# Kernel optimization log

Hardware: AMD Instinct MI355X
Metric: run time of the kernel (lower is better)

The kernel has to match this reference:

```python
import jax, jax.numpy as jnp
import numpy as np

CAUSAL = True


def setup_inputs() -> dict:
    key = jax.random.key(0)
    k1, k2, k3 = jax.random.split(key, 3)
    B, H, T, D = 2, 16, 2048, 64
    q = jax.random.normal(k1, (B, H, T, D), dtype=jnp.float32)
    k = jax.random.normal(k2, (B, H, T, D), dtype=jnp.float32)
    v = jax.random.normal(k3, (B, H, T, D), dtype=jnp.float32)
    return {"q": q, "k": k, "v": v}


def reference(q, k, v):
    # q,k,v: [B,H,T,D]
    d = q.shape[-1]
    scale = d ** -0.5
    dots = jnp.einsum('bhid,bhjd->bhij', q, k) * scale  # [B,H,T,T]
    if CAUSAL:
        t = q.shape[2]
        mask = jnp.triu(jnp.ones((t, t), dtype=bool), k=1)  # True above diagonal
        dots = jnp.where(mask, -jnp.inf, dots)
    attn = jax.nn.softmax(dots, axis=-1)
    # torch.einsum('bhjd,bhij->bhid', v, attn) == attn @ v
    return jnp.einsum('bhij,bhjd->bhid', attn, v)
```

## Files before the change

### kernel.cpp

```cpp
#include <hip/hip_runtime.h>
#include <hip/hip_bf16.h>

typedef unsigned short u16;
typedef unsigned int u32;
typedef __bf16 bf16x8 __attribute__((ext_vector_type(8)));
typedef short s16x4 __attribute__((ext_vector_type(4)));
typedef short s16x8 __attribute__((ext_vector_type(8)));
typedef float floatx4 __attribute__((ext_vector_type(4)));

#define T_SEQ 2048
#define HDIM 64
#define NBH 32

static __device__ __forceinline__ u16 f2b_rne(float x) {
    union { float f; u32 u; } c; c.f = x;
    u32 u = c.u;
    return (u16)((u + 0x7fffu + ((u >> 16) & 1u)) >> 16);
}
static __device__ __forceinline__ u16 f2b_trunc(float x) {
    union { float f; u32 u; } c; c.f = x;
    return (u16)(c.u >> 16);
}

#define GLOAD_LDS16(gp, lp)                                                      \
    __builtin_amdgcn_global_load_lds(                                            \
        (const __attribute__((address_space(1))) u32*)(gp),                      \
        (__attribute__((address_space(3))) u32*)(lp), 16, 0, 0)

__global__ __launch_bounds__(256) void prep(const float* __restrict__ k,
                                            const float* __restrict__ v,
                                            u16* __restrict__ kb,
                                            u16* __restrict__ vt) {
    __shared__ u16 tile[64][68];
    const int bh = blockIdx.y, t0 = blockIdx.x * 64;
    const int tid = threadIdx.x;

    const float* ksrc = k + ((size_t)bh * T_SEQ + t0) * HDIM;
    u16* kdst = kb + ((size_t)bh * T_SEQ + t0) * HDIM;
#pragma unroll
    for (int p = 0; p < 4; p++) {
        int idx = p * 256 + tid;
        float4 f = ((const float4*)ksrc)[idx];
        ushort4 o;
        o.x = f2b_rne(f.x); o.y = f2b_rne(f.y); o.z = f2b_rne(f.z); o.w = f2b_rne(f.w);
        ((ushort4*)kdst)[idx] = o;
    }

    const float* vsrc = v + ((size_t)bh * T_SEQ + t0) * HDIM;
#pragma unroll
    for (int p = 0; p < 4; p++) {
        int idx = p * 256 + tid;
        int r = idx >> 4, c4 = (idx & 15) * 4;
        float4 f = *(const float4*)(vsrc + r * HDIM + c4);
        tile[c4 + 0][r] = f2b_rne(f.x);
        tile[c4 + 1][r] = f2b_rne(f.y);
        tile[c4 + 2][r] = f2b_rne(f.z);
        tile[c4 + 3][r] = f2b_rne(f.w);
    }
    __syncthreads();
    u16* dst = vt + (size_t)bh * HDIM * T_SEQ + t0;
#pragma unroll
    for (int p = 0; p < 4; p++) {
        int idx = p * 256 + tid;
        int d = idx >> 4, c4 = (idx & 15) * 4;
        int win = c4 >> 5, kt = (c4 >> 4) & 1, qg = (c4 >> 2) & 3;
        int pos = win * 32 + qg * 8 + kt * 4;
        *(ushort4*)(dst + (size_t)d * T_SEQ + pos) = *(ushort4*)(&tile[d][c4]);
    }
}

__global__ __launch_bounds__(256, 2) void fattn(const float* __restrict__ q,
                                                const u16* __restrict__ kb,
                                                const u16* __restrict__ vtb,
                                                float* __restrict__ out) {
    __shared__ __align__(16) u16 smem[35328];

    const int bh = blockIdx.x;
    const int qt = 31 - (int)blockIdx.y;
    const int tid = threadIdx.x;
    const int wave = tid >> 6, lane = tid & 63;
    const int l15 = lane & 15, quad = lane >> 4;

    const float* qp = q + (size_t)bh * T_SEQ * HDIM;
    const u16* kp = kb + (size_t)bh * T_SEQ * HDIM;
    const u16* vp = vtb + (size_t)bh * HDIM * T_SEQ;

    const int nwin = 2 * qt + 2;
    const int nmy = (nwin > wave) ? ((nwin - wave + 3) >> 2) : 0;

    u16* Tb = smem + wave * 8192;

    const int ln3 = lane >> 3, ln7 = lane & 7;
    const int ln2 = lane >> 2, ln3m = lane & 3;

    auto stage = [&](int win, int b) {
        const u16* ks = kp + win * 32 * HDIM;
        u16* Kd = Tb + b * 2048;
#pragma unroll
        for (int l = 0; l < 4; l++) {
            int kr = l * 8 + ln3;
            GLOAD_LDS16(ks + kr * HDIM + (ln7 ^ (kr & 7)) * 8, Kd + l * 512);
        }
        const u16* vs = vp + win * 32;
        u16* Vd = Tb + 4096 + b * 2048;
#pragma unroll
        for (int l = 0; l < 4; l++) {
            int dr = l * 16 + ln2;
            GLOAD_LDS16(vs + (size_t)dr * T_SEQ + ((ln3m - dr) & 3) * 8, Vd + l * 512);
        }
    };

    const float SL2E = 0.125f * 1.44269504088896f;
    bf16x8 qf[4][2];
#pragma unroll
    for (int qn = 0; qn < 4; qn++) {
        const float* qrow = qp + (size_t)(qt * 64 + qn * 16 + l15) * HDIM;
#pragma unroll
        for (int kc = 0; kc < 2; kc++) {
            const float4* p4 = (const float4*)(qrow + kc * 32 + quad * 8);
            float4 fa = p4[0], fb = p4[1];
            union { bf16x8 v; u16 s[8]; } cv;
            cv.s[0] = f2b_rne(fa.x * SL2E); cv.s[1] = f2b_rne(fa.y * SL2E);
            cv.s[2] = f2b_rne(fa.z * SL2E); cv.s[3] = f2b_rne(fa.w * SL2E);
            cv.s[4] = f2b_rne(fb.x * SL2E); cv.s[5] = f2b_rne(fb.y * SL2E);
            cv.s[6] = f2b_rne(fb.z * SL2E); cv.s[7] = f2b_rne(fb.w * SL2E);
            qf[qn][kc] = cv.v;
        }
    }
    asm volatile("s_waitcnt vmcnt(0)" ::: "memory");

    if (nmy > 0) stage(wave, 0);
    if (nmy > 1) stage(wave + 4, 1);

    floatx4 o_acc[4][4];
#pragma unroll
    for (int qn = 0; qn < 4; qn++)
#pragma unroll
        for (int dt = 0; dt < 4; dt++) o_acc[qn][dt] = (floatx4){0.f, 0.f, 0.f, 0.f};
    float lsum[4] = {0.f, 0.f, 0.f, 0.f};

    for (int i = 0; i < nmy; i++) {
        const int win = wave + 4 * i;
        const int b = i & 1;
        if (i + 1 < nmy) { asm volatile("s_waitcnt vmcnt(8)" ::: "memory"); }
        else             { asm volatile("s_waitcnt vmcnt(0)" ::: "memory"); }

        const u16* Kc = Tb + b * 2048;
        bf16x8 kf[2][2];
#pragma unroll
        for (int kt = 0; kt < 2; kt++) {
            int kr = kt * 16 + l15;
#pragma unroll
            for (int kc = 0; kc < 2; kc++)
                kf[kt][kc] = *(const bf16x8*)(Kc + kr * 64 + (((kc * 4 + quad) ^ (kr & 7)) * 8));
        }
        const u16* Vc = Tb + 4096 + b * 2048;
        s16x8 vfull[4];
#pragma unroll
        for (int dt = 0; dt < 4; dt++) {
            int d = dt * 16 + l15;
            vfull[dt] = *(const s16x8*)(Vc + d * 32 + ((quad + d) & 3) * 8);
        }
        asm volatile("s_waitcnt lgkmcnt(0)" ::: "memory");
        if (i + 2 < nmy) stage(wave + 4 * (i + 2), b);

        floatx4 sacc[2][4];
#pragma unroll
        for (int kt = 0; kt < 2; kt++)
#pragma unroll
            for (int qn = 0; qn < 4; qn++) sacc[kt][qn] = (floatx4){0.f, 0.f, 0.f, 0.f};
#pragma unroll
        for (int kc = 0; kc < 2; kc++)
#pragma unroll
            for (int kt = 0; kt < 2; kt++)
#pragma unroll
                for (int qn = 0; qn < 4; qn++)
                    sacc[kt][qn] = __builtin_amdgcn_mfma_f32_16x16x32_bf16(
                        kf[kt][kc], qf[qn][kc], sacc[kt][qn], 0, 0, 0);

        s16x4 pf[2][4];
        if (win >= 2 * qt) {
            const int base = (win - 2 * qt) * 32;
#pragma unroll
            for (int kt = 0; kt < 2; kt++)
#pragma unroll
                for (int qn = 0; qn < 4; qn++) {
                    union { s16x4 v; u16 h[4]; } pk;
#pragma unroll
                    for (int rg = 0; rg < 4; rg++) {
                        float e = __builtin_amdgcn_exp2f(sacc[kt][qn][rg]);
                        if (base + kt * 16 + quad * 4 + rg > qn * 16 + l15) e = 0.f;
                        lsum[qn] += e;
                        pk.h[rg] = f2b_trunc(e);
                    }
                    pf[kt][qn] = pk.v;
                }
        } else {
#pragma unroll
            for (int kt = 0; kt < 2; kt++)
#pragma unroll
                for (int qn = 0; qn < 4; qn++) {
                    union { s16x4 v; u16 h[4]; } pk;
#pragma unroll
                    for (int rg = 0; rg < 4; rg++) {
                        float e = __builtin_amdgcn_exp2f(sacc[kt][qn][rg]);
                        lsum[qn] += e;
                        pk.h[rg] = f2b_trunc(e);
                    }
                    pf[kt][qn] = pk.v;
                }
        }

#pragma unroll
        for (int dt = 0; dt < 4; dt++) {
            s16x4 v0 = __builtin_shufflevector(vfull[dt], vfull[dt], 0, 1, 2, 3);
            s16x4 v1 = __builtin_shufflevector(vfull[dt], vfull[dt], 4, 5, 6, 7);
#pragma unroll
            for (int qn = 0; qn < 4; qn++) {
                o_acc[qn][dt] = __builtin_amdgcn_mfma_f32_16x16x16bf16_1k(pf[0][qn], v0, o_acc[qn][dt], 0, 0, 0);
                o_acc[qn][dt] = __builtin_amdgcn_mfma_f32_16x16x16bf16_1k(pf[1][qn], v1, o_acc[qn][dt], 0, 0, 0);
            }
        }
    }

    __syncthreads();
    float* oq = (float*)smem + wave * 4352;
#pragma unroll
    for (int qn = 0; qn < 4; qn++)
#pragma unroll
        for (int dt = 0; dt < 4; dt++)
#pragma unroll
            for (int rg = 0; rg < 4; rg++)
                oq[(qn * 16 + quad * 4 + rg) * 68 + dt * 16 + l15] = o_acc[qn][dt][rg];

    float* lsa = (float*)smem + 17408;
#pragma unroll
    for (int qn = 0; qn < 4; qn++) {
        float t = lsum[qn];
        t += __shfl_xor(t, 16, 64);
        t += __shfl_xor(t, 32, 64);
        if (quad == 0) lsa[wave * 64 + qn * 16 + l15] = t;
    }
    __syncthreads();

    {
        const int qr = wave * 16 + l15;
        float lt = lsa[qr] + lsa[64 + qr] + lsa[128 + qr] + lsa[192 + qr];
        float inv = 1.0f / lt;
        const float* q0 = (float*)smem + qr * 68 + quad * 16;
        float* op = out + ((size_t)bh * T_SEQ + qt * 64 + qr) * HDIM + quad * 16;
#pragma unroll
        for (int c = 0; c < 4; c++) {
            float4 s0 = *(const float4*)(q0 + c * 4);
            float4 s1 = *(const float4*)(q0 + 4352 + c * 4);
            float4 s2 = *(const float4*)(q0 + 8704 + c * 4);
            float4 s3 = *(const float4*)(q0 + 13056 + c * 4);
            float4 r;
            r.x = (s0.x + s1.x + s2.x + s3.x) * inv;
            r.y = (s0.y + s1.y + s2.y + s3.y) * inv;
            r.z = (s0.z + s1.z + s2.z + s3.z) * inv;
            r.w = (s0.w + s1.w + s2.w + s3.w) * inv;
            *(float4*)(op + c * 4) = r;
        }
    }
}

extern "C" void kernel_launch(void* const* d_in, const int* in_sizes, int n_in,
                              void* d_out, int out_size, void* d_ws, size_t ws_size,
                              hipStream_t stream) {
    const float* q = (const float*)d_in[0];
    const float* k = (const float*)d_in[1];
    const float* v = (const float*)d_in[2];
    float* out = (float*)d_out;

    u16* kb = (u16*)d_ws;
    u16* vt = kb + (size_t)NBH * T_SEQ * HDIM;

    prep<<<dim3(T_SEQ / 64, NBH), 256, 0, stream>>>(k, v, kb, vt);
    fattn<<<dim3(NBH, 32), 256, 0, stream>>>(q, kb, vt, out);
}
```

Baseline: 124.2 us.

## Shrink per-wave KV windows to 16 keys and cut LDS for higher occupancy

```diff
diff --git a/kernel.cpp b/kernel.cpp
--- a/kernel.cpp
+++ b/kernel.cpp
@@ -5,7 +5,6 @@
 typedef unsigned int u32;
 typedef __bf16 bf16x8 __attribute__((ext_vector_type(8)));
 typedef short s16x4 __attribute__((ext_vector_type(4)));
-typedef short s16x8 __attribute__((ext_vector_type(8)));
 typedef float floatx4 __attribute__((ext_vector_type(4)));
 
 #define T_SEQ 2048
@@ -17,9 +16,9 @@
     u32 u = c.u;
     return (u16)((u + 0x7fffu + ((u >> 16) & 1u)) >> 16);
 }
-static __device__ __forceinline__ u16 f2b_trunc(float x) {
+static __device__ __forceinline__ u32 fbits(float x) {
     union { float f; u32 u; } c; c.f = x;
-    return (u16)(c.u >> 16);
+    return c.u;
 }
 
 #define GLOAD_LDS16(gp, lp)                                                      \
@@ -63,17 +62,15 @@
     for (int p = 0; p < 4; p++) {
         int idx = p * 256 + tid;
         int d = idx >> 4, c4 = (idx & 15) * 4;
-        int win = c4 >> 5, kt = (c4 >> 4) & 1, qg = (c4 >> 2) & 3;
-        int pos = win * 32 + qg * 8 + kt * 4;
-        *(ushort4*)(dst + (size_t)d * T_SEQ + pos) = *(ushort4*)(&tile[d][c4]);
-    }
-}
-
-__global__ __launch_bounds__(256, 2) void fattn(const float* __restrict__ q,
+        *(ushort4*)(dst + (size_t)d * T_SEQ + c4) = *(ushort4*)(&tile[d][c4]);
+    }
+}
+
+__global__ __launch_bounds__(256, 3) void fattn(const float* __restrict__ q,
                                                 const u16* __restrict__ kb,
                                                 const u16* __restrict__ vtb,
                                                 float* __restrict__ out) {
-    __shared__ __align__(16) u16 smem[35328];
+    __shared__ __align__(16) u16 smem[18944];
 
     const int bh = blockIdx.x;
     const int qt = 31 - (int)blockIdx.y;
@@ -85,29 +82,22 @@
     const u16* kp = kb + (size_t)bh * T_SEQ * HDIM;
     const u16* vp = vtb + (size_t)bh * HDIM * T_SEQ;
 
-    const int nwin = 2 * qt + 2;
-    const int nmy = (nwin > wave) ? ((nwin - wave + 3) >> 2) : 0;
-
-    u16* Tb = smem + wave * 8192;
-
-    const int ln3 = lane >> 3, ln7 = lane & 7;
-    const int ln2 = lane >> 2, ln3m = lane & 3;
+    u16* Tb = smem + wave * 4096;
+
+    const int kr = lane >> 3;
+    const u16* kg0 = kp + kr * HDIM + ((lane & 7) ^ (kr & 7)) * 8;
+    const int vdr = lane >> 1;
+    const u16* vg0 = vp + (size_t)vdr * T_SEQ + (((lane & 1) + (vdr >> 2)) & 1) * 8;
 
     auto stage = [&](int win, int b) {
-        const u16* ks = kp + win * 32 * HDIM;
-        u16* Kd = Tb + b * 2048;
-#pragma unroll
-        for (int l = 0; l < 4; l++) {
-            int kr = l * 8 + ln3;
-            GLOAD_LDS16(ks + kr * HDIM + (ln7 ^ (kr & 7)) * 8, Kd + l * 512);
-        }
-        const u16* vs = vp + win * 32;
-        u16* Vd = Tb + 4096 + b * 2048;
-#pragma unroll
-        for (int l = 0; l < 4; l++) {
-            int dr = l * 16 + ln2;
-            GLOAD_LDS16(vs + (size_t)dr * T_SEQ + ((ln3m - dr) & 3) * 8, Vd + l * 512);
-        }
+        const u16* ks = kg0 + win * 16 * HDIM;
+        u16* Kd = Tb + b * 1024;
+        GLOAD_LDS16(ks, Kd);
+        GLOAD_LDS16(ks + 8 * HDIM, Kd + 512);
+        const u16* vs = vg0 + win * 16;
+        u16* Vd = Tb + 2048 + b * 1024;
+        GLOAD_LDS16(vs, Vd);
+        GLOAD_LDS16(vs + (size_t)32 * T_SEQ, Vd + 512);
     };
 
     const float SL2E = 0.125f * 1.44269504088896f;
@@ -129,8 +119,8 @@
     }
     asm volatile("s_waitcnt vmcnt(0)" ::: "memory");
 
-    if (nmy > 0) stage(wave, 0);
-    if (nmy > 1) stage(wave + 4, 1);
+    stage(wave, 0);
+    if (qt >= 1) stage(wave + 4, 1);
 
     floatx4 o_acc[4][4];
 #pragma unroll
@@ -138,102 +128,87 @@
 #pragma unroll
         for (int dt = 0; dt < 4; dt++) o_acc[qn][dt] = (floatx4){0.f, 0.f, 0.f, 0.f};
     float lsum[4] = {0.f, 0.f, 0.f, 0.f};
-
-    for (int i = 0; i < nmy; i++) {
-        const int win = wave + 4 * i;
+    const floatx4 ZERO4 = {0.f, 0.f, 0.f, 0.f};
+    const int vph = ((quad >> 1) + (l15 >> 2)) & 1;
+
+    for (int i = 0; i <= qt; ++i) {
         const int b = i & 1;
-        if (i + 1 < nmy) { asm volatile("s_waitcnt vmcnt(8)" ::: "memory"); }
-        else             { asm volatile("s_waitcnt vmcnt(0)" ::: "memory"); }
-
-        const u16* Kc = Tb + b * 2048;
-        bf16x8 kf[2][2];
-#pragma unroll
-        for (int kt = 0; kt < 2; kt++) {
-            int kr = kt * 16 + l15;
-#pragma unroll
-            for (int kc = 0; kc < 2; kc++)
-                kf[kt][kc] = *(const bf16x8*)(Kc + kr * 64 + (((kc * 4 + quad) ^ (kr & 7)) * 8));
-        }
-        const u16* Vc = Tb + 4096 + b * 2048;
-        s16x8 vfull[4];
-#pragma unroll
-        for (int dt = 0; dt < 4; dt++) {
-            int d = dt * 16 + l15;
-            vfull[dt] = *(const s16x8*)(Vc + d * 32 + ((quad + d) & 3) * 8);
-        }
+        if (i < qt) { asm volatile("s_waitcnt vmcnt(4)" ::: "memory"); }
+        else        { asm volatile("s_waitcnt vmcnt(0)" ::: "memory"); }
+
+        const u16* Kc = Tb + b * 1024;
+        bf16x8 kf0 = *(const bf16x8*)(Kc + l15 * 64 + ((quad) ^ (l15 & 7)) * 8);
+        bf16x8 kf1 = *(const bf16x8*)(Kc + l15 * 64 + ((4 + quad) ^ (l15 & 7)) * 8);
+        const u16* Vc = Tb + 2048 + b * 1024;
+        s16x4 vf[4];
+#pragma unroll
+        for (int dt = 0; dt < 4; dt++)
+            vf[dt] = *(const s16x4*)(Vc + (dt * 16 + l15) * 16 + vph * 8 + (quad & 1) * 4);
         asm volatile("s_waitcnt lgkmcnt(0)" ::: "memory");
-        if (i + 2 < nmy) stage(wave + 4 * (i + 2), b);
-
-        floatx4 sacc[2][4];
-#pragma unroll
-        for (int kt = 0; kt < 2; kt++)
-#pragma unroll
-            for (int qn = 0; qn < 4; qn++) sacc[kt][qn] = (floatx4){0.f, 0.f, 0.f, 0.f};
-#pragma unroll
-        for (int kc = 0; kc < 2; kc++)
-#pragma unroll
-            for (int kt = 0; kt < 2; kt++)
-#pragma unroll
-                for (int qn = 0; qn < 4; qn++)
-                    sacc[kt][qn] = __builtin_amdgcn_mfma_f32_16x16x32_bf16(
-                        kf[kt][kc], qf[qn][kc], sacc[kt][qn], 0, 0, 0);
-
-        s16x4 pf[2][4];
-        if (win >= 2 * qt) {
-            const int base = (win - 2 * qt) * 32;
-#pragma unroll
-            for (int kt = 0; kt < 2; kt++)
-#pragma unroll
-                for (int qn = 0; qn < 4; qn++) {
-                    union { s16x4 v; u16 h[4]; } pk;
-#pragma unroll
-                    for (int rg = 0; rg < 4; rg++) {
-                        float e = __builtin_amdgcn_exp2f(sacc[kt][qn][rg]);
-                        if (base + kt * 16 + quad * 4 + rg > qn * 16 + l15) e = 0.f;
-                        lsum[qn] += e;
-                        pk.h[rg] = f2b_trunc(e);
-                    }
-                    pf[kt][qn] = pk.v;
-                }
+        if (i + 2 <= qt) stage(wave + 4 * (i + 2), b);
+
+        floatx4 sacc[4];
+#pragma unroll
+        for (int qn = 0; qn < 4; qn++)
+            sacc[qn] = __builtin_amdgcn_mfma_f32_16x16x32_bf16(kf0, qf[qn][0], ZERO4, 0, 0, 0);
+#pragma unroll
+        for (int qn = 0; qn < 4; qn++)
+            sacc[qn] = __builtin_amdgcn_mfma_f32_16x16x32_bf16(kf1, qf[qn][1], sacc[qn], 0, 0, 0);
+
+        s16x4 pf[4];
+        if (i == qt) {
+#pragma unroll
+            for (int qn = 0; qn < 4; qn++) {
+                const int rhs = qn * 16 + l15;
+                float e0 = __builtin_amdgcn_exp2f(sacc[qn][0]);
+                float e1 = __builtin_amdgcn_exp2f(sacc[qn][1]);
+                float e2 = __builtin_amdgcn_exp2f(sacc[qn][2]);
+                float e3 = __builtin_amdgcn_exp2f(sacc[qn][3]);
+                if (wave * 16 + quad * 4 + 0 > rhs) e0 = 0.f;
+                if (wave * 16 + quad * 4 + 1 > rhs) e1 = 0.f;
+                if (wave * 16 + quad * 4 + 2 > rhs) e2 = 0.f;
+                if (wave * 16 + quad * 4 + 3 > rhs) e3 = 0.f;
+                lsum[qn] += (e0 + e1) + (e2 + e3);
+                union { s16x4 v; u32 w[2]; } pk;
+                pk.w[0] = __builtin_amdgcn_perm(fbits(e1), fbits(e0), 0x07060302u);
+                pk.w[1] = __builtin_amdgcn_perm(fbits(e3), fbits(e2), 0x07060302u);
+                pf[qn] = pk.v;
+            }
         } else {
 #pragma unroll
-            for (int kt = 0; kt < 2; kt++)
-#pragma unroll
-                for (int qn = 0; qn < 4; qn++) {
-                    union { s16x4 v; u16 h[4]; } pk;
-#pragma unroll
-                    for (int rg = 0; rg < 4; rg++) {
-                        float e = __builtin_amdgcn_exp2f(sacc[kt][qn][rg]);
-                        lsum[qn] += e;
-                        pk.h[rg] = f2b_trunc(e);
-                    }
-                    pf[kt][qn] = pk.v;
-                }
-        }
-
-#pragma unroll
-        for (int dt = 0; dt < 4; dt++) {
-            s16x4 v0 = __builtin_shufflevector(vfull[dt], vfull[dt], 0, 1, 2, 3);
-            s16x4 v1 = __builtin_shufflevector(vfull[dt], vfull[dt], 4, 5, 6, 7);
-#pragma unroll
             for (int qn = 0; qn < 4; qn++) {
-                o_acc[qn][dt] = __builtin_amdgcn_mfma_f32_16x16x16bf16_1k(pf[0][qn], v0, o_acc[qn][dt], 0, 0, 0);
-                o_acc[qn][dt] = __builtin_amdgcn_mfma_f32_16x16x16bf16_1k(pf[1][qn], v1, o_acc[qn][dt], 0, 0, 0);
+                float e0 = __builtin_amdgcn_exp2f(sacc[qn][0]);
+                float e1 = __builtin_amdgcn_exp2f(sacc[qn][1]);
+                float e2 = __builtin_amdgcn_exp2f(sacc[qn][2]);
+                float e3 = __builtin_amdgcn_exp2f(sacc[qn][3]);
+                lsum[qn] += (e0 + e1) + (e2 + e3);
+                union { s16x4 v; u32 w[2]; } pk;
+                pk.w[0] = __builtin_amdgcn_perm(fbits(e1), fbits(e0), 0x07060302u);
+                pk.w[1] = __builtin_amdgcn_perm(fbits(e3), fbits(e2), 0x07060302u);
+                pf[qn] = pk.v;
             }
         }
+
+#pragma unroll
+        for (int qn = 0; qn < 4; qn++)
+#pragma unroll
+            for (int dt = 0; dt < 4; dt++)
+                o_acc[qn][dt] = __builtin_amdgcn_mfma_f32_16x16x16bf16_1k(
+                    pf[qn], vf[dt], o_acc[qn][dt], 0, 0, 0);
     }
 
     __syncthreads();
-    float* oq = (float*)smem + wave * 4352;
+    u16* ob = smem + wave * 4608;
 #pragma unroll
     for (int qn = 0; qn < 4; qn++)
 #pragma unroll
         for (int dt = 0; dt < 4; dt++)
 #pragma unroll
             for (int rg = 0; rg < 4; rg++)
-                oq[(qn * 16 + quad * 4 + rg) * 68 + dt * 16 + l15] = o_acc[qn][dt][rg];
-
-    float* lsa = (float*)smem + 17408;
+                ob[(qn * 16 + quad * 4 + rg) * 72 + dt * 16 + l15] =
+                    f2b_rne(o_acc[qn][dt][rg]);
+
+    float* lsa = (float*)(smem + 18432);
 #pragma unroll
     for (int qn = 0; qn < 4; qn++) {
         float t = lsum[qn];
@@ -247,19 +222,32 @@
         const int qr = wave * 16 + l15;
         float lt = lsa[qr] + lsa[64 + qr] + lsa[128 + qr] + lsa[192 + qr];
         float inv = 1.0f / lt;
-        const float* q0 = (float*)smem + qr * 68 + quad * 16;
+        float acc[16];
+#pragma unroll
+        for (int x = 0; x < 16; x++) acc[x] = 0.f;
+#pragma unroll
+        for (int w4 = 0; w4 < 4; w4++) {
+            const u16* pb = smem + w4 * 4608 + qr * 72 + quad * 16;
+            uint4 a = *(const uint4*)(pb);
+            uint4 b2 = *(const uint4*)(pb + 8);
+            u32 w[8] = {a.x, a.y, a.z, a.w, b2.x, b2.y, b2.z, b2.w};
+#pragma unroll
+            for (int e = 0; e < 8; e++) {
+                union { u32 u; float f; } lo, hi;
+                lo.u = w[e] << 16;
+                hi.u = w[e] & 0xffff0000u;
+                acc[e * 2] += lo.f;
+                acc[e * 2 + 1] += hi.f;
+            }
+        }
         float* op = out + ((size_t)bh * T_SEQ + qt * 64 + qr) * HDIM + quad * 16;
 #pragma unroll
         for (int c = 0; c < 4; c++) {
-            float4 s0 = *(const float4*)(q0 + c * 4);
-            float4 s1 = *(const float4*)(q0 + 4352 + c * 4);
-            float4 s2 = *(const float4*)(q0 + 8704 + c * 4);
-            float4 s3 = *(const float4*)(q0 + 13056 + c * 4);
             float4 r;
-            r.x = (s0.x + s1.x + s2.x + s3.x) * inv;
-            r.y = (s0.y + s1.y + s2.y + s3.y) * inv;
-            r.z = (s0.z + s1.z + s2.z + s3.z) * inv;
-            r.w = (s0.w + s1.w + s2.w + s3.w) * inv;
+            r.x = acc[c * 4 + 0] * inv;
+            r.y = acc[c * 4 + 1] * inv;
+            r.z = acc[c * 4 + 2] * inv;
+            r.w = acc[c * 4 + 3] * inv;
             *(float4*)(op + c * 4) = r;
         }
     }
```

Result: slower. 127.4 us (+2.5%).
